# Optimization experiments

Measured on AMD Instinct MI355X. Metric: run time of the kernel, lower is better.

Reference implementation:

```python
import jax, jax.numpy as jnp
import numpy as np

B, S, D = 4, 2048, 2048
H = 16
HD = D // H  # head_dim = 128


def setup_inputs() -> dict:
    key = jax.random.key(0)
    ks = jax.random.split(key, 6)
    x = jax.random.normal(ks[0], (B, S, D), dtype=jnp.float32)
    Wq = jax.random.normal(ks[1], (D, D), dtype=jnp.float32) * 0.02
    Wk = jax.random.normal(ks[2], (D, D), dtype=jnp.float32) * 0.02
    Wv = jax.random.normal(ks[3], (D, D), dtype=jnp.float32) * 0.02
    Wo = jax.random.normal(ks[4], (D, D), dtype=jnp.float32) * 0.02
    bo = jax.random.normal(ks[5], (D,), dtype=jnp.float32) * 0.02
    return {"x": x, "Wq": Wq, "Wk": Wk, "Wv": Wv, "Wo": Wo, "bo": bo}


def reference(x, Wq, Wk, Wv, Wo, bo):
    b, s, _ = x.shape
    # QKV projections, split heads: [b, h, s, hd]
    q = (x @ Wq).reshape(b, s, H, HD).transpose(0, 2, 1, 3)
    k = (x @ Wk).reshape(b, s, H, HD).transpose(0, 2, 1, 3)
    v = (x @ Wv).reshape(b, s, H, HD).transpose(0, 2, 1, 3)
    # scores: [b, h, s_q, s_k]
    scores = jnp.einsum("bhqd,bhkd->bhqk", q, k)
    # causal mask: future positions (k > q) get -inf (masking before scaling,
    # as in the original; -inf is invariant under the scale)
    causal = jnp.tril(jnp.ones((s, s), dtype=bool))
    scores = jnp.where(causal, scores, -jnp.inf)
    scale = 1.0 / np.sqrt(HD).astype(np.float32)
    attn = jax.nn.softmax(scores * scale, axis=-1)
    # dropout p=0.0 -> identity (eval-mode reference)
    ctx = jnp.einsum("bhqk,bhkd->bqhd", attn, v).reshape(b, s, D)
    return ctx @ Wo + bo
```

## Files before the change

kernel.cpp:

```cpp
#include <hip/hip_runtime.h>
#include <hip/hip_bf16.h>

#define BB 4
#define SS 2048
#define DD 2048
#define HH 16
#define HDD 128

typedef __bf16 bf16x8_t __attribute__((ext_vector_type(8)));
typedef float f32x4 __attribute__((ext_vector_type(4)));
typedef float f32x16 __attribute__((ext_vector_type(16)));

static __device__ __forceinline__ unsigned short f2bf(float f) {
    union { float f; unsigned u; } v; v.f = f;
    unsigned r = v.u + 0x7fffu + ((v.u >> 16) & 1u);
    return (unsigned short)(r >> 16);
}

static __device__ __forceinline__ unsigned cvtpk_bf16(float lo, float hiv) {
    unsigned r;
    asm("v_cvt_pk_bf16_f32 %0, %1, %2" : "=v"(r) : "v"(lo), "v"(hiv));
    return r;
}

static __device__ __forceinline__ void pl32swap(unsigned& a, unsigned& b) {
    auto rr = __builtin_amdgcn_permlane32_swap((int)a, (int)b, false, false);
    a = (unsigned)rr[0];
    b = (unsigned)rr[1];
}

static __device__ __forceinline__ void gload_lds16(const void* g, void* lds) {
    __builtin_amdgcn_global_load_lds(
        (const __attribute__((address_space(1))) void*)g,
        (__attribute__((address_space(3))) void*)lds, 16, 0, 0);
}

__global__ void convert_x(const float* __restrict__ x, unsigned short* __restrict__ xb, int n) {
    int i = (blockIdx.x * blockDim.x + threadIdx.x) * 4;
    int stride = gridDim.x * blockDim.x * 4;
    for (; i < n; i += stride) {
        float4 v = *(const float4*)(x + i);
        ushort4 o;
        o.x = f2bf(v.x); o.y = f2bf(v.y); o.z = f2bf(v.z); o.w = f2bf(v.w);
        *(ushort4*)(xb + i) = o;
    }
}

__global__ void transpose_w(const float* __restrict__ Wq, const float* __restrict__ Wk,
                            const float* __restrict__ Wv, const float* __restrict__ Wo,
                            unsigned short* __restrict__ WqkvT, unsigned short* __restrict__ WoT) {
    __shared__ float t[32][33];
    const int z = blockIdx.z;
    const float* W = (z == 0) ? Wq : (z == 1) ? Wk : (z == 2) ? Wv : Wo;
    unsigned short* T = (z < 3) ? (WqkvT + (size_t)z * DD * DD) : WoT;
    const int k0 = blockIdx.x * 32, n0 = blockIdx.y * 32;
    const int tx = threadIdx.x, ty = threadIdx.y;
#pragma unroll
    for (int i = 0; i < 4; ++i) {
        int r = ty + i * 8;
        t[r][tx] = W[(size_t)(k0 + r) * DD + n0 + tx];
    }
    __syncthreads();
#pragma unroll
    for (int i = 0; i < 4; ++i) {
        int r = ty + i * 8;
        T[(size_t)(n0 + r) * DD + k0 + tx] = f2bf(t[tx][r]);
    }
}

template <int MODE>
__global__ __launch_bounds__(512, 1) void gemm256(
    const unsigned short* __restrict__ A, const unsigned short* __restrict__ BT,
    unsigned short* __restrict__ outQ, unsigned short* __restrict__ outK,
    unsigned short* __restrict__ outV, float* __restrict__ outF,
    const float* __restrict__ bias) {
    __shared__ __attribute__((aligned(16))) char lds[131072];
    const int tid = threadIdx.x, l = tid & 63;
    const int w = tid >> 6;
    const int wr = w >> 2, wc = w & 3;
    const int nwg = gridDim.x * gridDim.y;
    int lin = blockIdx.y * gridDim.x + blockIdx.x;
    lin = (lin & 7) * (nwg >> 3) + (lin >> 3);
    const int m0 = (lin / gridDim.x) * 256;
    const int n0 = (lin % gridDim.x) * 256;

    f32x4 acc[8][4] = {};

    const int rowl = tid >> 3, c16s = tid & 7;
    const int sw16 = (c16s ^ (rowl & 7)) * 16;
    const char* aSrc[4];
    const char* bSrc[4];
#pragma unroll
    for (int rg = 0; rg < 4; ++rg) {
        aSrc[rg] = (const char*)A + ((size_t)(m0 + rg * 64 + rowl) * 2048) * 2 + sw16;
        bSrc[rg] = (const char*)BT + ((size_t)(n0 + rg * 64 + rowl) * 2048) * 2 + sw16;
    }
    const int dstOff = tid * 16;

    auto stage2 = [&](int slot, int off, int which) {
        char* sA = lds + slot * 32768;
        char* sB = lds + 65536 + slot * 32768;
        if (which == 0) { gload_lds16(bSrc[0] + off, sB + 0 * 8192 + dstOff); gload_lds16(bSrc[1] + off, sB + 1 * 8192 + dstOff); }
        else if (which == 1) { gload_lds16(bSrc[2] + off, sB + 2 * 8192 + dstOff); gload_lds16(bSrc[3] + off, sB + 3 * 8192 + dstOff); }
        else if (which == 2) { gload_lds16(aSrc[0] + off, sA + 0 * 8192 + dstOff); gload_lds16(aSrc[2] + off, sA + 2 * 8192 + dstOff); }
        else { gload_lds16(aSrc[1] + off, sA + 1 * 8192 + dstOff); gload_lds16(aSrc[3] + off, sA + 3 * 8192 + dstOff); }
    };

#pragma unroll
    for (int q = 0; q < 4; ++q) stage2(0, 0, q);
    asm volatile("s_waitcnt vmcnt(0)" ::: "memory");
    __builtin_amdgcn_s_barrier();

    const int lr = l & 15, hi4 = l >> 4;
    for (int t = 0; t < 32; ++t) {
        const int cur = t & 1, sl1 = cur ^ 1;
        const bool nlast = (t + 1 < 32);
        const int off1 = (t + 1) * 128;
        const char* As_ = lds + cur * 32768;
        const char* Bs_ = lds + 65536 + cur * 32768;
        bf16x8_t aa[4], bb[4];

#pragma unroll
        for (int mq = 0; mq < 4; ++mq) {
            int row = wr * 128 + mq * 16 + lr;
            aa[mq] = *(const bf16x8_t*)(As_ + row * 128 + ((hi4) ^ (row & 7)) * 16);
        }
#pragma unroll
        for (int nq = 0; nq < 4; ++nq) {
            int col = wc * 64 + nq * 16 + lr;
            bb[nq] = *(const bf16x8_t*)(Bs_ + col * 128 + ((hi4) ^ (col & 7)) * 16);
        }
        if (nlast) stage2(sl1, off1, 0);
        __builtin_amdgcn_s_barrier();
        asm volatile("s_waitcnt lgkmcnt(0)");
        __builtin_amdgcn_s_setprio(1);
#pragma unroll
        for (int mq = 0; mq < 4; ++mq)
#pragma unroll
            for (int nq = 0; nq < 4; ++nq)
                acc[mq][nq] = __builtin_amdgcn_mfma_f32_16x16x32_bf16(aa[mq], bb[nq], acc[mq][nq], 0, 0, 0);
        __builtin_amdgcn_s_setprio(0);
        if (nlast) { asm volatile("s_waitcnt vmcnt(2)" ::: "memory"); }
        else       { asm volatile("s_waitcnt vmcnt(0)" ::: "memory"); }
        __builtin_amdgcn_s_barrier();

#pragma unroll
        for (int mq = 0; mq < 4; ++mq) {
            int row = wr * 128 + 64 + mq * 16 + lr;
            aa[mq] = *(const bf16x8_t*)(As_ + row * 128 + ((hi4) ^ (row & 7)) * 16);
        }
        if (nlast) stage2(sl1, off1, 1);
        __builtin_amdgcn_s_barrier();
        asm volatile("s_waitcnt lgkmcnt(0)");
        __builtin_amdgcn_s_setprio(1);
#pragma unroll
        for (int mq = 0; mq < 4; ++mq)
#pragma unroll
            for (int nq = 0; nq < 4; ++nq)
                acc[4 + mq][nq] = __builtin_amdgcn_mfma_f32_16x16x32_bf16(aa[mq], bb[nq], acc[4 + mq][nq], 0, 0, 0);
        __builtin_amdgcn_s_setprio(0);
        __builtin_amdgcn_s_barrier();

#pragma unroll
        for (int mq = 0; mq < 4; ++mq) {
            int row = wr * 128 + mq * 16 + lr;
            aa[mq] = *(const bf16x8_t*)(As_ + row * 128 + ((4 + hi4) ^ (row & 7)) * 16);
        }
#pragma unroll
        for (int nq = 0; nq < 4; ++nq) {
            int col = wc * 64 + nq * 16 + lr;
            bb[nq] = *(const bf16x8_t*)(Bs_ + col * 128 + ((4 + hi4) ^ (col & 7)) * 16);
        }
        if (nlast) stage2(sl1, off1, 2);
        __builtin_amdgcn_s_barrier();
        asm volatile("s_waitcnt lgkmcnt(0)");
        __builtin_amdgcn_s_setprio(1);
#pragma unroll
        for (int mq = 0; mq < 4; ++mq)
#pragma unroll
            for (int nq = 0; nq < 4; ++nq)
                acc[mq][nq] = __builtin_amdgcn_mfma_f32_16x16x32_bf16(aa[mq], bb[nq], acc[mq][nq], 0, 0, 0);
        __builtin_amdgcn_s_setprio(0);
        __builtin_amdgcn_s_barrier();

#pragma unroll
        for (int mq = 0; mq < 4; ++mq) {
            int row = wr * 128 + 64 + mq * 16 + lr;
            aa[mq] = *(const bf16x8_t*)(As_ + row * 128 + ((4 + hi4) ^ (row & 7)) * 16);
        }
        if (nlast) stage2(sl1, off1, 3);
        __builtin_amdgcn_s_barrier();
        asm volatile("s_waitcnt lgkmcnt(0)");
        __builtin_amdgcn_s_setprio(1);
#pragma unroll
        for (int mq = 0; mq < 4; ++mq)
#pragma unroll
            for (int nq = 0; nq < 4; ++nq)
                acc[4 + mq][nq] = __builtin_amdgcn_mfma_f32_16x16x32_bf16(aa[mq], bb[nq], acc[4 + mq][nq], 0, 0, 0);
        __builtin_amdgcn_s_setprio(0);
        if (nlast) { asm volatile("s_waitcnt vmcnt(2)" ::: "memory"); }
        __builtin_amdgcn_s_barrier();
    }

    const int rbase = m0 + wr * 128 + (hi4 << 2);
    const int cbase = n0 + wc * 64 + lr;
    if (MODE == 0) {
#pragma unroll
        for (int nq = 0; nq < 4; ++nq) {
            int col = cbase + nq * 16;
            int mat = col >> 11;
            int nn = col & 2047;
            int h = nn >> 7, hd = nn & 127;
            if (mat == 2) {
#pragma unroll
                for (int i = 0; i < 8; ++i) {
                    int row = rbase + i * 16;
                    int b = row >> 11, s = row & 2047;
                    ushort4 pk;
                    pk.x = f2bf(acc[i][nq][0]); pk.y = f2bf(acc[i][nq][1]);
                    pk.z = f2bf(acc[i][nq][2]); pk.w = f2bf(acc[i][nq][3]);
                    *(ushort4*)(outV + ((size_t)(b * HH + h) * HDD + hd) * SS + s) = pk;
                }
            } else {
                unsigned short* outp = mat ? outK : outQ;
#pragma unroll
                for (int i = 0; i < 8; ++i) {
#pragma unroll
                    for (int r = 0; r < 4; ++r) {
                        int row = rbase + i * 16 + r;
                        int b = row >> 11, s = row & 2047;
                        outp[((size_t)(b * HH + h) * SS + s) * HDD + hd] = f2bf(acc[i][nq][r]);
                    }
                }
            }
        }
    } else {
#pragma unroll
        for (int nq = 0; nq < 4; ++nq) {
            int col = cbase + nq * 16;
            float bv = bias[col];
#pragma unroll
            for (int i = 0; i < 8; ++i) {
#pragma unroll
                for (int r = 0; r < 4; ++r) {
                    int row = rbase + i * 16 + r;
                    outF[(size_t)row * DD + col] = acc[i][nq][r] + bv;
                }
            }
        }
    }
}

__global__ __launch_bounds__(256, 2) void attn_kernel(
    const unsigned short* __restrict__ Q, const unsigned short* __restrict__ K,
    const unsigned short* __restrict__ VT, unsigned short* __restrict__ ctx) {
    __shared__ __attribute__((aligned(16))) unsigned short Ks[2][64 * 128];
    __shared__ __attribute__((aligned(16))) unsigned short Vs[2][128 * 64];
    __shared__ float Al[4][32];
    const int tid = threadIdx.x, w = tid >> 6, l = tid & 63;
    const int hi = l >> 5, l31 = l & 31;
    const int hb = hi * 16;
    const int swzK = (l31 & 15) << 4;
    const int swzV = (l31 & 7) << 4;
    const int p = blockIdx.x, h = blockIdx.y, b = blockIdx.z;
    const int bh = b * HH + h;
    const float scale2 = 0.08838834764831845f * 1.4426950408889634f;

    const unsigned short* Qbh = Q + (size_t)bh * SS * HDD;
    const char* Kbh = (const char*)(K + (size_t)bh * SS * HDD);
    const char* Vbh = (const char*)(VT + (size_t)bh * HDD * SS);

    const char* kbase[4];
    const char* vbase[4];
#pragma unroll
    for (int i = 0; i < 4; ++i) {
        int cp = (i * 256 + tid) * 16;
        int krow = cp >> 8, kcb = cp & 255;
        kbase[i] = Kbh + (size_t)krow * 256 + (kcb ^ ((krow & 15) << 4));
        int vrow = cp >> 7, vcb = cp & 127;
        vbase[i] = Vbh + (size_t)vrow * (SS * 2) + (vcb ^ ((vrow & 7) << 4));
    }

    auto stage = [&](int buf, int kv0) {
#pragma unroll
        for (int i = 0; i < 4; ++i) {
            int cp = (i * 256 + tid) * 16;
            gload_lds16(kbase[i] + (size_t)kv0 * 256, (char*)&Ks[buf][0] + cp);
            gload_lds16(vbase[i] + (size_t)kv0 * 2, (char*)&Vs[buf][0] + cp);
        }
    };

    for (int pass = 0; pass < 2; ++pass) {
        const int qt = pass ? p : 15 - p;
        const int q0w = qt * 128 + w * 32;
        const int qabs = q0w + l31;
        const int nkv = 2 * qt + 2;

        bf16x8_t qf[8];
#pragma unroll
        for (int ds = 0; ds < 8; ++ds)
            qf[ds] = *(const bf16x8_t*)(Qbh + (size_t)qabs * HDD + ds * 16 + hi * 8);

        float m_r = -1e30f, l_r = 0.f;
        f32x16 o0 = {}, o1 = {}, o2 = {}, o3 = {};

        int buf = 0;
        stage(0, 0);
        __syncthreads();

        for (int kt = 0; kt < nkv; ++kt) {
            const int kv0 = kt * 64;
            if (kt + 1 < nkv) stage(buf ^ 1, kv0 + 64);

            if (kv0 <= q0w + 31) {
                const char* Kb = (const char*)&Ks[buf][0];
                const char* Vb = (const char*)&Vs[buf][0];
                f32x16 s0 = {}, s1 = {};
                {
                    bf16x8_t kf[8];
                    const int rb = l31 * 256;
#pragma unroll
                    for (int ds = 0; ds < 8; ++ds)
                        kf[ds] = *(const bf16x8_t*)(Kb + rb + ((ds * 32 + hb) ^ swzK));
                    __builtin_amdgcn_s_setprio(1);
#pragma unroll
                    for (int ds = 0; ds < 8; ++ds)
                        s0 = __builtin_amdgcn_mfma_f32_32x32x16_bf16(kf[ds], qf[ds], s0, 0, 0, 0);
                    __builtin_amdgcn_s_setprio(0);
#pragma unroll
                    for (int ds = 0; ds < 8; ++ds)
                        kf[ds] = *(const bf16x8_t*)(Kb + rb + 32 * 256 + ((ds * 32 + hb) ^ swzK));
                    __builtin_amdgcn_s_setprio(1);
#pragma unroll
                    for (int ds = 0; ds < 8; ++ds)
                        s1 = __builtin_amdgcn_mfma_f32_32x32x16_bf16(kf[ds], qf[ds], s1, 0, 0, 0);
                    __builtin_amdgcn_s_setprio(0);
                }

                if (kv0 + 63 > q0w) {
                    const int qrel = qabs - kv0;
#pragma unroll
                    for (int r = 0; r < 16; ++r) {
                        const int kl = (r & 3) + 8 * (r >> 2) + 4 * hi;
                        s0[r] = (kl > qrel) ? -1e30f : s0[r] * scale2;
                        s1[r] = (kl + 32 > qrel) ? -1e30f : s1[r] * scale2;
                    }
                } else {
#pragma unroll
                    for (int r = 0; r < 16; ++r) { s0[r] *= scale2; s1[r] *= scale2; }
                }

                float mx = s0[0];
#pragma unroll
                for (int r = 1; r < 16; ++r) mx = fmaxf(mx, s0[r]);
#pragma unroll
                for (int r = 0; r < 16; ++r) mx = fmaxf(mx, s1[r]);
                {
                    unsigned mu = __float_as_uint(mx), mu2 = mu;
                    pl32swap(mu, mu2);
                    mx = fmaxf(__uint_as_float(mu), __uint_as_float(mu2));
                }

                if (__any(mx - m_r > 8.f)) {
                    float mnew = fmaxf(m_r, mx);
                    float alpha = exp2f(m_r - mnew);
                    m_r = mnew;
                    l_r *= alpha;
                    Al[w][l31] = alpha;
#pragma unroll
                    for (int r = 0; r < 16; ++r) {
                        float ar = Al[w][(r & 3) + 8 * (r >> 2) + 4 * hi];
                        o0[r] *= ar; o1[r] *= ar; o2[r] *= ar; o3[r] *= ar;
                    }
                }

                float ps = 0.f;
#pragma unroll
                for (int r = 0; r < 16; ++r) { s0[r] = exp2f(s0[r] - m_r); ps += s0[r]; }
#pragma unroll
                for (int r = 0; r < 16; ++r) { s1[r] = exp2f(s1[r] - m_r); ps += s1[r]; }
                {
                    unsigned pu = __float_as_uint(ps), pu2 = pu;
                    pl32swap(pu, pu2);
                    l_r += __uint_as_float(pu) + __uint_as_float(pu2);
                }

                bf16x8_t pa[4];
                {
                    union { unsigned u[4]; bf16x8_t v; } uu;
#define MK_PA(SV, BASE, OUT)                                     \
                    {                                            \
                        unsigned X0 = cvtpk_bf16(SV[BASE + 0], SV[BASE + 1]); \
                        unsigned Y0 = cvtpk_bf16(SV[BASE + 4], SV[BASE + 5]); \
                        pl32swap(X0, Y0);                        \
                        unsigned X1 = cvtpk_bf16(SV[BASE + 2], SV[BASE + 3]); \
                        unsigned Y1 = cvtpk_bf16(SV[BASE + 6], SV[BASE + 7]); \
                        pl32swap(X1, Y1);                        \
                        uu.u[0] = X0; uu.u[1] = X1; uu.u[2] = Y0; uu.u[3] = Y1; \
                        OUT = uu.v;                              \
                    }
                    MK_PA(s0, 0, pa[0]);
                    MK_PA(s0, 8, pa[1]);
                    MK_PA(s1, 0, pa[2]);
                    MK_PA(s1, 8, pa[3]);
#undef MK_PA
                }

#pragma unroll
                for (int ks = 0; ks < 4; ++ks) {
                    bf16x8_t vf[4];
#pragma unroll
                    for (int dsub = 0; dsub < 4; ++dsub)
                        vf[dsub] = *(const bf16x8_t*)(Vb + (dsub * 32 + l31) * 128 + ((ks * 32 + hb) ^ swzV));
                    __builtin_amdgcn_s_setprio(1);
                    o0 = __builtin_amdgcn_mfma_f32_32x32x16_bf16(pa[ks], vf[0], o0, 0, 0, 0);
                    o1 = __builtin_amdgcn_mfma_f32_32x32x16_bf16(pa[ks], vf[1], o1, 0, 0, 0);
                    o2 = __builtin_amdgcn_mfma_f32_32x32x16_bf16(pa[ks], vf[2], o2, 0, 0, 0);
                    o3 = __builtin_amdgcn_mfma_f32_32x32x16_bf16(pa[ks], vf[3], o3, 0, 0, 0);
                    __builtin_amdgcn_s_setprio(0);
                }
            }
            __syncthreads();
            buf ^= 1;
        }

        Al[w][l31] = 1.f / l_r;
        unsigned short* cb_ = ctx + (size_t)b * SS * DD + (size_t)h * HDD;
#pragma unroll
        for (int r = 0; r < 16; ++r) {
            const int ql = (r & 3) + 8 * (r >> 2) + 4 * hi;
            float inv = Al[w][ql];
            const size_t rowoff = (size_t)(q0w + ql) * DD;
            cb_[rowoff + 0 * 32 + l31] = f2bf(o0[r] * inv);
            cb_[rowoff + 1 * 32 + l31] = f2bf(o1[r] * inv);
            cb_[rowoff + 2 * 32 + l31] = f2bf(o2[r] * inv);
            cb_[rowoff + 3 * 32 + l31] = f2bf(o3[r] * inv);
        }
    }
}

extern "C" void kernel_launch(void* const* d_in, const int* in_sizes, int n_in,
                              void* d_out, int out_size, void* d_ws, size_t ws_size,
                              hipStream_t stream) {
    (void)in_sizes; (void)n_in; (void)out_size; (void)ws_size;
    const float* x  = (const float*)d_in[0];
    const float* Wq = (const float*)d_in[1];
    const float* Wk = (const float*)d_in[2];
    const float* Wv = (const float*)d_in[3];
    const float* Wo = (const float*)d_in[4];
    const float* bo = (const float*)d_in[5];

    char* ws = (char*)d_ws;
    unsigned short* xb    = (unsigned short*)(ws);
    unsigned short* WqkvT = (unsigned short*)(ws + (32u << 20));
    unsigned short* WoT   = (unsigned short*)(ws + (56u << 20));
    unsigned short* Qb    = (unsigned short*)(ws + (64u << 20));
    unsigned short* Kb    = (unsigned short*)(ws + (96u << 20));
    unsigned short* VTb   = (unsigned short*)(ws + (160u << 20));
    unsigned short* ctx   = xb;

    convert_x<<<4096, 256, 0, stream>>>(x, xb, BB * SS * DD);
    transpose_w<<<dim3(64, 64, 4), dim3(32, 8), 0, stream>>>(Wq, Wk, Wv, Wo, WqkvT, WoT);
    gemm256<0><<<dim3(24, 32), 512, 0, stream>>>(xb, WqkvT, Qb, Kb, VTb, nullptr, nullptr);
    attn_kernel<<<dim3(8, HH, BB), 256, 0, stream>>>(Qb, Kb, VTb, ctx);
    gemm256<1><<<dim3(8, 32), 512, 0, stream>>>(ctx, WoT, nullptr, nullptr, nullptr, (float*)d_out, bo);
}
```

Measured before the change: 425.0 us.

## Fold softmax scale into Q projection and split K/V waits in attention loop

The QKV projection epilogue now multiplies Q by the softmax scale times log2(e) before the bf16 store, so the attention kernel no longer scales scores each tile. The attention loop replaces the single __syncthreads with fine-grained vmcnt waits and raw barriers: it waits only for the K tile before QK^T and for the V tile before PV, so V loads can overlap the softmax. This adds more barriers per iteration and relies on the exact count of outstanding loads, and rounding Q to bf16 after scaling slightly changes numerics.

```diff
diff --git a/kernel.cpp b/kernel.cpp
--- a/kernel.cpp
+++ b/kernel.cpp
@@ -205,6 +205,7 @@
     const int rbase = m0 + wr * 128 + (hi4 << 2);
     const int cbase = n0 + wc * 64 + lr;
     if (MODE == 0) {
+        const float QSCALE = 0.08838834764831845f * 1.4426950408889634f;
 #pragma unroll
         for (int nq = 0; nq < 4; ++nq) {
             int col = cbase + nq * 16;
@@ -223,13 +224,14 @@
                 }
             } else {
                 unsigned short* outp = mat ? outK : outQ;
+                const float sc = mat ? 1.f : QSCALE;
 #pragma unroll
                 for (int i = 0; i < 8; ++i) {
 #pragma unroll
                     for (int r = 0; r < 4; ++r) {
                         int row = rbase + i * 16 + r;
                         int b = row >> 11, s = row & 2047;
-                        outp[((size_t)(b * HH + h) * SS + s) * HDD + hd] = f2bf(acc[i][nq][r]);
+                        outp[((size_t)(b * HH + h) * SS + s) * HDD + hd] = f2bf(acc[i][nq][r] * sc);
                     }
                 }
             }
@@ -264,7 +266,6 @@
     const int swzV = (l31 & 7) << 4;
     const int p = blockIdx.x, h = blockIdx.y, b = blockIdx.z;
     const int bh = b * HH + h;
-    const float scale2 = 0.08838834764831845f * 1.4426950408889634f;
 
     const unsigned short* Qbh = Q + (size_t)bh * SS * HDD;
     const char* Kbh = (const char*)(K + (size_t)bh * SS * HDD);
@@ -281,11 +282,17 @@
         vbase[i] = Vbh + (size_t)vrow * (SS * 2) + (vcb ^ ((vrow & 7) << 4));
     }
 
-    auto stage = [&](int buf, int kv0) {
+    auto stageK = [&](int buf, int kv0) {
 #pragma unroll
         for (int i = 0; i < 4; ++i) {
             int cp = (i * 256 + tid) * 16;
             gload_lds16(kbase[i] + (size_t)kv0 * 256, (char*)&Ks[buf][0] + cp);
+        }
+    };
+    auto stageV = [&](int buf, int kv0) {
+#pragma unroll
+        for (int i = 0; i < 4; ++i) {
+            int cp = (i * 256 + tid) * 16;
             gload_lds16(vbase[i] + (size_t)kv0 * 2, (char*)&Vs[buf][0] + cp);
         }
     };
@@ -305,17 +312,23 @@
         f32x16 o0 = {}, o1 = {}, o2 = {}, o3 = {};
 
         int buf = 0;
-        stage(0, 0);
-        __syncthreads();
+        stageK(0, 0);
+        stageV(0, 0);
+        asm volatile("s_waitcnt vmcnt(4)" ::: "memory");
+        __builtin_amdgcn_s_barrier();
 
         for (int kt = 0; kt < nkv; ++kt) {
             const int kv0 = kt * 64;
-            if (kt + 1 < nkv) stage(buf ^ 1, kv0 + 64);
-
-            if (kv0 <= q0w + 31) {
-                const char* Kb = (const char*)&Ks[buf][0];
-                const char* Vb = (const char*)&Vs[buf][0];
-                f32x16 s0 = {}, s1 = {};
+            const bool nlast = (kt + 1 < nkv);
+            if (nlast) { stageK(buf ^ 1, kv0 + 64); stageV(buf ^ 1, kv0 + 64); }
+
+            const bool active = (kv0 <= q0w + 31);
+            const char* Kb = (const char*)&Ks[buf][0];
+            const char* Vb = (const char*)&Vs[buf][0];
+            f32x16 s0, s1;
+            bf16x8_t pa[4];
+            if (active) {
+                s0 = (f32x16){}; s1 = (f32x16){};
                 {
                     bf16x8_t kf[8];
                     const int rb = l31 * 256;
@@ -342,12 +355,9 @@
 #pragma unroll
                     for (int r = 0; r < 16; ++r) {
                         const int kl = (r & 3) + 8 * (r >> 2) + 4 * hi;
-                        s0[r] = (kl > qrel) ? -1e30f : s0[r] * scale2;
-                        s1[r] = (kl + 32 > qrel) ? -1e30f : s1[r] * scale2;
+                        if (kl > qrel) s0[r] = -1e30f;
+                        if (kl + 32 > qrel) s1[r] = -1e30f;
                     }
-                } else {
-#pragma unroll
-                    for (int r = 0; r < 16; ++r) { s0[r] *= scale2; s1[r] *= scale2; }
                 }
 
                 float mx = s0[0];
@@ -385,7 +395,6 @@
                     l_r += __uint_as_float(pu) + __uint_as_float(pu2);
                 }
 
-                bf16x8_t pa[4];
                 {
                     union { unsigned u[4]; bf16x8_t v; } uu;
 #define MK_PA(SV, BASE, OUT)                                     \
@@ -405,7 +414,13 @@
                     MK_PA(s1, 8, pa[3]);
 #undef MK_PA
                 }
-
+            }
+
+            if (nlast) { asm volatile("s_waitcnt vmcnt(8)" ::: "memory"); }
+            else       { asm volatile("s_waitcnt vmcnt(0)" ::: "memory"); }
+            __builtin_amdgcn_s_barrier();
+
+            if (active) {
 #pragma unroll
                 for (int ks = 0; ks < 4; ++ks) {
                     bf16x8_t vf[4];
@@ -420,7 +435,9 @@
                     __builtin_amdgcn_s_setprio(0);
                 }
             }
-            __syncthreads();
+
+            if (nlast) { asm volatile("s_waitcnt vmcnt(4)" ::: "memory"); }
+            __builtin_amdgcn_s_barrier();
             buf ^= 1;
         }
 
@@ -436,6 +453,7 @@
             cb_[rowoff + 2 * 32 + l31] = f2bf(o2[r] * inv);
             cb_[rowoff + 3 * 32 + l31] = f2bf(o3[r] * inv);
         }
+        __syncthreads();
     }
 }
 
```

Measured after the change: 427.5 us. No clear change (+0.6%).
